# Kernel optimization log

Measured on AMD Instinct MI355X. Metric: run time of the kernel, lower is better.

## Reference

```python
import jax, jax.numpy as jnp
import numpy as np

B, S = 1, 2560
DIM, NH, HD = 1536, 12, 128
F, HH, WW = 4, 20, 32        # F*HH*WW == S (video latent grid)
EPS = 1e-6
C = HD // 2                  # 64 rotary pairs per head
TD = C - 2 * (C // 3)        # 22 temporal rotary dims
SD = C // 3                  # 21 spatial rotary dims (h and w each)


def setup_inputs() -> dict:
    key = jax.random.key(0)
    ks = jax.random.split(key, 4)
    x = jax.random.normal(ks[0], (B, S, DIM), jnp.float32)
    # Wan-style 3D RoPE angle table: angle[pos, j] = pos * inv_freq_j,
    # segments [0:TD]=temporal, [TD:TD+SD]=height, [TD+SD:]=width.
    def inv(n):
        return 1.0 / (10000.0 ** (np.arange(n, dtype=np.float64) / n))
    inv_full = np.concatenate([inv(TD), inv(SD), inv(SD)])
    freqs = jnp.asarray(np.arange(1024)[:, None] * inv_full[None, :], jnp.float32)
    seq_lens = jnp.full((B,), S, jnp.int32)
    grid_sizes = jnp.asarray([[F, HH, WW]], jnp.int32)
    Wqkv = jax.random.normal(ks[1], (DIM, 3 * DIM), jnp.float32) * 0.02
    bqkv = jnp.zeros((3 * DIM,), jnp.float32)
    gq = jnp.ones((DIM,), jnp.float32)
    gk = jnp.ones((DIM,), jnp.float32)
    Wo = jax.random.normal(ks[2], (DIM, DIM), jnp.float32) * 0.02
    bo = jnp.zeros((DIM,), jnp.float32)
    return dict(x=x, seq_lens=seq_lens, grid_sizes=grid_sizes, freqs=freqs,
                Wqkv=Wqkv, bqkv=bqkv, gq=gq, gk=gk, Wo=Wo, bo=bo)


def _rms(x, g):
    xf = x.astype(jnp.float32)
    y = xf * jax.lax.rsqrt(jnp.mean(xf * xf, axis=-1, keepdims=True) + EPS)
    return (y * g).astype(x.dtype)


def _rope3d(x, freqs):
    # x: [B,S,NH,HD]; rotate adjacent (even,odd) pairs by grid-position angles.
    idx = jnp.arange(S)
    f = idx // (HH * WW)
    h = (idx // WW) % HH
    w = idx % WW
    ang = jnp.concatenate([freqs[f, :TD], freqs[h, TD:TD + SD], freqs[w, TD + SD:]], axis=-1)  # [S, C]
    cos = jnp.cos(ang)[None, :, None, :]
    sin = jnp.sin(ang)[None, :, None, :]
    xr, xi = x[..., 0::2], x[..., 1::2]
    out = jnp.stack([xr * cos - xi * sin, xr * sin + xi * cos], axis=-1)
    return out.reshape(x.shape)


def reference(x, seq_lens, grid_sizes, freqs, Wqkv, bqkv, gq, gk, Wo, bo):
    qkv = x @ Wqkv + bqkv                              # [B,S,3*DIM]
    q, k, v = jnp.split(qkv, 3, axis=-1)
    q = _rms(q, gq).reshape(B, S, NH, HD)
    k = _rms(k, gk).reshape(B, S, NH, HD)
    v = v.reshape(B, S, NH, HD)
    q = _rope3d(q, freqs)
    k = _rope3d(k, freqs)
    scores = jnp.einsum('bsnd,btnd->bnst', q, k) / jnp.sqrt(jnp.float32(HD))
    kmask = (jnp.arange(S)[None, :] < seq_lens[:, None])[:, None, None, :]  # k_lens masking
    scores = jnp.where(kmask, scores, jnp.float32(-1e30))
    attn = jax.nn.softmax(scores, axis=-1)
    out = jnp.einsum('bnst,btnd->bsnd', attn, v).reshape(B, S, DIM)
    return out @ Wo + bo
```

## Files before the change

kernel.cpp:

```cpp
#include <hip/hip_runtime.h>
#include <hip/hip_bf16.h>

constexpr int Sq  = 2560;
constexpr int Dm  = 1536;
constexpr int NHe = 12;
constexpr int HDim= 128;
constexpr int N3c = 4608;
constexpr int TDc = 22;
constexpr int SDc = 21;
constexpr int HHc = 20;
constexpr int WWc = 32;

typedef __attribute__((ext_vector_type(4)))  float f32x4;
typedef __attribute__((ext_vector_type(16))) float f32x16;
typedef __attribute__((ext_vector_type(8)))  short bf16x8;
typedef __attribute__((ext_vector_type(4)))  unsigned u32x4;

__device__ __forceinline__ short f2bf(float f) {
  __hip_bfloat16 h = __float2bfloat16(f);
  return __builtin_bit_cast(short, h);
}
__device__ __forceinline__ float bf2f(short s) {
  __hip_bfloat16 h = __builtin_bit_cast(__hip_bfloat16, s);
  return __bfloat162float(h);
}
__device__ __forceinline__ void gll16(const void* g, void* l) {
  __builtin_amdgcn_global_load_lds((const __attribute__((address_space(1))) unsigned int*)g,
                                   (__attribute__((address_space(3))) unsigned int*)l, 16, 0, 0);
}
__device__ __forceinline__ unsigned cvtpk(float lo, float hi) {
  unsigned r;
  asm("v_cvt_pk_bf16_f32 %0, %1, %2" : "=v"(r) : "v"(lo), "v"(hi));
  return r;
}

__global__ __launch_bounds__(256) void k_convert(const float* __restrict__ in,
                                                 short* __restrict__ out, int n4) {
  int i = blockIdx.x * 256 + threadIdx.x;
  if (i >= n4) return;
  float4 v = reinterpret_cast<const float4*>(in)[i];
  short4 o;
  o.x = f2bf(v.x); o.y = f2bf(v.y); o.z = f2bf(v.z); o.w = f2bf(v.w);
  reinterpret_cast<short4*>(out)[i] = o;
}

__global__ void k_transpose_cvt(const float* __restrict__ in, short* __restrict__ out,
                                int R, int C_) {
  __shared__ float tile[32][33];
  int c0 = blockIdx.x * 32, r0 = blockIdx.y * 32;
  int tx = threadIdx.x, ty = threadIdx.y;
#pragma unroll
  for (int i = 0; i < 4; ++i)
    tile[ty + i * 8][tx] = in[(size_t)(r0 + ty + i * 8) * C_ + c0 + tx];
  __syncthreads();
#pragma unroll
  for (int i = 0; i < 4; ++i)
    out[(size_t)(c0 + ty + i * 8) * R + r0 + tx] = f2bf(tile[tx][ty + i * 8]);
}

__global__ void k_transpose_bf16(const short* __restrict__ in, short* __restrict__ out,
                                 int R, int C_) {
  __shared__ short tile[32][34];
  int h = blockIdx.z;
  const short* ih = in + (size_t)h * R * C_;
  short* oh = out + (size_t)h * R * C_;
  int c0 = blockIdx.x * 32, r0 = blockIdx.y * 32;
  int tx = threadIdx.x, ty = threadIdx.y;
#pragma unroll
  for (int i = 0; i < 4; ++i)
    tile[ty + i * 8][tx] = ih[(size_t)(r0 + ty + i * 8) * C_ + c0 + tx];
  __syncthreads();
#pragma unroll
  for (int i = 0; i < 4; ++i)
    oh[(size_t)(c0 + ty + i * 8) * R + r0 + tx] = tile[tx][ty + i * 8];
}

template <int OUT_BF16, int BM, int NTMAJOR>
__global__ __launch_bounds__(256) void k_gemm_bt(const short* __restrict__ A,
                                                 const short* __restrict__ BT,
                                                 const float* __restrict__ bias,
                                                 void* __restrict__ Cp,
                                                 int M, int N, int K, int den) {
  constexpr int MF = BM / 32;
  __shared__ short As[2 * BM * 32];
  __shared__ short Bs[2 * 128 * 32];
  int cpx = gridDim.x >> 3;
  int bid = (blockIdx.x & 7) * cpx + (blockIdx.x >> 3);
  int mt, nt;
  if (NTMAJOR) { mt = bid % den; nt = bid / den; }
  else         { mt = bid / den; nt = bid % den; }
  int tid = threadIdx.x, lane = tid & 63, wid = tid >> 6;
  int wr = wid >> 1, wc = wid & 1;
  f32x4 zero = {0.f, 0.f, 0.f, 0.f};
  f32x4 acc[MF][4];
#pragma unroll
  for (int m = 0; m < MF; ++m)
#pragma unroll
    for (int n = 0; n < 4; ++n) acc[m][n] = zero;

  int lrow = lane >> 2;
  int lk8 = (lane & 3) * 8;
  const size_t arow0 = (size_t)mt * BM, brow0 = (size_t)nt * 128;
  int la = lane & 15, lg = lane >> 4;

  for (int kk = 0; kk < K; kk += 64) {
#pragma unroll
    for (int h = 0; h < 2; ++h) {
#pragma unroll
      for (int i = 0; i < MF / 2; ++i) {
        int rA = (wid * (MF / 2) + i) * 16 + lrow;
        gll16(A + (arow0 + rA) * K + kk + h * 32 + lk8,
              As + h * BM * 32 + rA * 32 + lk8);
      }
#pragma unroll
      for (int i = 0; i < 2; ++i) {
        int rB = (wid * 2 + i) * 16 + lrow;
        gll16(BT + (brow0 + rB) * K + kk + h * 32 + lk8,
              Bs + h * 128 * 32 + rB * 32 + lk8);
      }
    }
    __syncthreads();
#pragma unroll
    for (int h = 0; h < 2; ++h) {
      bf16x8 af[MF], bfr[4];
#pragma unroll
      for (int m = 0; m < MF; ++m)
        af[m] = *(const bf16x8*)(As + h * BM * 32 + (wr * (BM / 2) + m * 16 + la) * 32 + lg * 8);
#pragma unroll
      for (int n = 0; n < 4; ++n)
        bfr[n] = *(const bf16x8*)(Bs + h * 128 * 32 + (wc * 64 + n * 16 + la) * 32 + lg * 8);
#pragma unroll
      for (int m = 0; m < MF; ++m)
#pragma unroll
        for (int n = 0; n < 4; ++n)
          acc[m][n] = __builtin_amdgcn_mfma_f32_16x16x32_bf16(af[m], bfr[n], acc[m][n], 0, 0, 0);
    }
    __syncthreads();
  }
#pragma unroll
  for (int m = 0; m < MF; ++m) {
    int r = (int)arow0 + wr * (BM / 2) + m * 16 + lg * 4;
#pragma unroll
    for (int n = 0; n < 4; ++n) {
      int c = (int)brow0 + wc * 64 + n * 16 + la;
      float b = bias[c];
#pragma unroll
      for (int i = 0; i < 4; ++i) {
        float v = acc[m][n][i] + b;
        if (OUT_BF16) ((short*)Cp)[(size_t)(r + i) * N + c] = f2bf(v);
        else          ((float*)Cp)[(size_t)(r + i) * N + c] = v;
      }
    }
  }
}

__global__ __launch_bounds__(256) void k_rmsrope(const short* __restrict__ qkv,
                                                 const float* __restrict__ freqs,
                                                 const float* __restrict__ gq,
                                                 const float* __restrict__ gk,
                                                 short* __restrict__ Q,
                                                 short* __restrict__ Kx,
                                                 short* __restrict__ V) {
  int s = blockIdx.x;
  const short* row = qkv + (size_t)s * N3c;
  __shared__ float cs[64], sn[64];
  __shared__ float wred[8];
  __shared__ float inv_s[2];
  int tid = threadIdx.x;
  if (tid < 64) {
    int f = s / (HHc * WWc), hh = (s / WWc) % HHc, ww = s % WWc;
    int ridx = tid < TDc ? f : (tid < TDc + SDc ? hh : ww);
    float ang = freqs[ridx * 64 + tid];
    cs[tid] = cosf(ang);
    sn[tid] = sinf(ang);
  }
  float sq = 0.f, sk = 0.f;
  if (tid < 192) {
    bf16x8 a = *(const bf16x8*)(row + tid * 8);
    bf16x8 b = *(const bf16x8*)(row + Dm + tid * 8);
#pragma unroll
    for (int j = 0; j < 8; ++j) {
      float fa = bf2f(a[j]); sq += fa * fa;
      float fb = bf2f(b[j]); sk += fb * fb;
    }
  }
#pragma unroll
  for (int o = 32; o > 0; o >>= 1) { sq += __shfl_down(sq, o); sk += __shfl_down(sk, o); }
  if ((tid & 63) == 0) { wred[tid >> 6] = sq; wred[4 + (tid >> 6)] = sk; }
  __syncthreads();
  if (tid == 0) {
    float a = wred[0] + wred[1] + wred[2] + wred[3];
    float b = wred[4] + wred[5] + wred[6] + wred[7];
    inv_s[0] = rsqrtf(a * (1.0f / Dm) + 1e-6f);
    inv_s[1] = rsqrtf(b * (1.0f / Dm) + 1e-6f);
  }
  __syncthreads();
  float invq = inv_s[0], invk = inv_s[1];
  const float qscale = 0.12751763f;
  for (int p = tid; p < NHe * 64; p += 256) {
    int hd = p >> 6, i = p & 63;
    float c = cs[i], sn_ = sn[i];
    int col = hd * HDim + 2 * i;
    size_t obase = ((size_t)hd * Sq + s) * HDim + 2 * i;
    float xr = bf2f(row[col])     * invq * gq[col];
    float xi = bf2f(row[col + 1]) * invq * gq[col + 1];
    Q[obase]     = f2bf((xr * c - xi * sn_) * qscale);
    Q[obase + 1] = f2bf((xr * sn_ + xi * c) * qscale);
    float yr = bf2f(row[Dm + col])     * invk * gk[col];
    float yi = bf2f(row[Dm + col + 1]) * invk * gk[col + 1];
    Kx[obase]     = f2bf(yr * c - yi * sn_);
    Kx[obase + 1] = f2bf(yr * sn_ + yi * c);
    V[obase]     = row[2 * Dm + col];
    V[obase + 1] = row[2 * Dm + col + 1];
  }
}

__global__ __launch_bounds__(256, 2) void k_attn(const short* __restrict__ Q,
                                                 const short* __restrict__ Kg,
                                                 const short* __restrict__ VT,
                                                 short* __restrict__ O) {
  __shared__ short Xb[2][64 * 128];
  __shared__ short Yb[2][64 * 128];
  __shared__ float Lsh[4][32];
  constexpr int NT = (Sq / 2) / 64;
  int bid = (blockIdx.x & 7) * 60 + (blockIdx.x >> 3);
  int h = bid / 40;
  int q0 = (bid % 40) * 64;
  int tid = threadIdx.x, lane = tid & 63, wid = tid >> 6;
  int qw = wid & 1, kw = wid >> 1;
  int la = lane & 31, hi = lane >> 5;
  const short* Qh = Q  + (size_t)h * Sq * HDim;
  const short* Kh = Kg + (size_t)h * Sq * HDim;
  const short* Vh = VT + (size_t)h * HDim * Sq;
  int qb = q0 + qw * 32;
  int tz = kw * (Sq / 2);
  short* X = Xb[kw];
  short* Y = Yb[kw];

  int koff[8], voff[8], ldo[8];
  const short* Kt = Kh + (size_t)tz * HDim;
  const short* Vt = Vh + tz;
#pragma unroll
  for (int i = 0; i < 8; ++i) {
    int off = (qw * 8 + i) * 1024 + lane * 16;
    int r  = off >> 8, cb  = off & 255;
    koff[i] = r * HDim + ((cb ^ ((r & 15) << 4)) >> 1);
    int r2 = off >> 7, cb2 = off & 127;
    voff[i] = r2 * Sq + ((cb2 ^ ((r2 & 7) << 4)) >> 1);
    ldo[i] = off >> 1;
  }
  auto stageK = [&]() {
#pragma unroll
    for (int i = 0; i < 8; ++i) gll16(Kt + koff[i], X + ldo[i]);
    Kt += 64 * HDim;
  };
  auto stageV = [&]() {
#pragma unroll
    for (int i = 0; i < 8; ++i) gll16(Vt + voff[i], Y + ldo[i]);
    Vt += 64;
  };

  stageK();

  bf16x8 qf[8];
#pragma unroll
  for (int dc = 0; dc < 8; ++dc)
    qf[dc] = *(const bf16x8*)(Qh + (size_t)(qb + la) * HDim + dc * 16 + hi * 8);

  f32x16 o0, o1, o2, o3;
#pragma unroll
  for (int r = 0; r < 16; ++r) { o0[r] = 0.f; o1[r] = 0.f; o2[r] = 0.f; o3[r] = 0.f; }
  float lsum = 0.f;
  const float M2 = 11.5415603f;

  __syncthreads();

  for (int t = 0; t < NT; ++t) {
    stageV();

    f32x16 s0, s1;
#pragma unroll
    for (int r = 0; r < 16; ++r) { s0[r] = 0.f; s1[r] = 0.f; }
    int kcb = ((la & 15) << 4);
#pragma unroll
    for (int dc = 0; dc < 8; ++dc) {
      int bc = (dc * 32 + hi * 16) ^ kcb;
      bf16x8 k0 = *(const bf16x8*)(X + la * 128 + (bc >> 1));
      bf16x8 k1 = *(const bf16x8*)(X + (32 + la) * 128 + (bc >> 1));
      s0 = __builtin_amdgcn_mfma_f32_32x32x16_bf16(k0, qf[dc], s0, 0, 0, 0);
      s1 = __builtin_amdgcn_mfma_f32_32x32x16_bf16(k1, qf[dc], s1, 0, 0, 0);
    }

    float p0[16], p1[16];
#pragma unroll
    for (int r = 0; r < 16; ++r) { p0[r] = exp2f(s0[r] - M2); p1[r] = exp2f(s1[r] - M2); }
    float a0 = 0.f, a1 = 0.f, a2 = 0.f, a3 = 0.f;
#pragma unroll
    for (int m = 0; m < 4; ++m) {
      a0 += p0[m]; a1 += p0[4 + m]; a2 += p0[8 + m]; a3 += p0[12 + m];
      a0 += p1[m]; a1 += p1[4 + m]; a2 += p1[8 + m]; a3 += p1[12 + m];
    }
    lsum += (a0 + a1) + (a2 + a3);

    unsigned w0[8], w1[8];
#pragma unroll
    for (int m = 0; m < 8; ++m) {
      w0[m] = cvtpk(p0[2 * m], p0[2 * m + 1]);
      w1[m] = cvtpk(p1[2 * m], p1[2 * m + 1]);
    }
    unsigned paw[4][4];
#pragma unroll
    for (int tcl = 0; tcl < 2; ++tcl)
#pragma unroll
      for (int jl = 0; jl < 2; ++jl) {
        unsigned A0 = w0[4 * tcl + jl], B0 = w0[4 * tcl + 2 + jl];
        asm("v_permlane32_swap_b32 %0, %1" : "+v"(A0), "+v"(B0));
        paw[tcl][jl] = A0; paw[tcl][2 + jl] = B0;
        unsigned A1 = w1[4 * tcl + jl], B1 = w1[4 * tcl + 2 + jl];
        asm("v_permlane32_swap_b32 %0, %1" : "+v"(A1), "+v"(B1));
        paw[2 + tcl][jl] = A1; paw[2 + tcl][2 + jl] = B1;
      }
    bf16x8 pa[4];
#pragma unroll
    for (int tc = 0; tc < 4; ++tc) {
      u32x4 tw = {paw[tc][0], paw[tc][1], paw[tc][2], paw[tc][3]};
      pa[tc] = __builtin_bit_cast(bf16x8, tw);
    }

    __syncthreads();

    if (t + 1 < NT) stageK();

    int vcb = ((la & 7) << 4);
#pragma unroll
    for (int tc = 0; tc < 4; ++tc) {
      int bc = (tc * 32 + hi * 16) ^ vcb;
      bf16x8 vf0 = *(const bf16x8*)(Y + (la)      * 64 + (bc >> 1));
      bf16x8 vf1 = *(const bf16x8*)(Y + (32 + la) * 64 + (bc >> 1));
      bf16x8 vf2 = *(const bf16x8*)(Y + (64 + la) * 64 + (bc >> 1));
      bf16x8 vf3 = *(const bf16x8*)(Y + (96 + la) * 64 + (bc >> 1));
      o0 = __builtin_amdgcn_mfma_f32_32x32x16_bf16(pa[tc], vf0, o0, 0, 0, 0);
      o1 = __builtin_amdgcn_mfma_f32_32x32x16_bf16(pa[tc], vf1, o1, 0, 0, 0);
      o2 = __builtin_amdgcn_mfma_f32_32x32x16_bf16(pa[tc], vf2, o2, 0, 0, 0);
      o3 = __builtin_amdgcn_mfma_f32_32x32x16_bf16(pa[tc], vf3, o3, 0, 0, 0);
    }
    __syncthreads();
  }

  {
    float A = lsum, B = lsum;
    asm("v_permlane32_swap_b32 %0, %1" : "+v"(A), "+v"(B));
    lsum = A + B;
  }
  if (hi == 0) Lsh[wid][la] = lsum;
  float* fb = (float*)(&Xb[0][0]);
  if (kw == 1) {
    float* dst = fb + qw * 4096 + lane;
#pragma unroll
    for (int r = 0; r < 16; ++r) {
      dst[(r)      * 64] = o0[r];
      dst[(16 + r) * 64] = o1[r];
      dst[(32 + r) * 64] = o2[r];
      dst[(48 + r) * 64] = o3[r];
    }
  }
  __syncthreads();
  if (kw == 0) {
    float ltot = lsum + Lsh[wid + 2][la];
    float rinv = 1.0f / ltot;
    if (hi == 0) Lsh[wid][la] = rinv;
    const float* src = fb + qw * 4096 + lane;
#pragma unroll
    for (int r = 0; r < 16; ++r) {
      o0[r] += src[(r)      * 64];
      o1[r] += src[(16 + r) * 64];
      o2[r] += src[(32 + r) * 64];
      o3[r] += src[(48 + r) * 64];
    }
    float rv[16];
#pragma unroll
    for (int r = 0; r < 16; ++r)
      rv[r] = Lsh[wid][(r & 3) + 8 * (r >> 2) + 4 * hi];
#pragma unroll
    for (int r = 0; r < 16; ++r) {
      int qrow = qb + (r & 3) + 8 * (r >> 2) + 4 * hi;
      short* orow = O + (size_t)qrow * Dm + h * HDim + la;
      orow[0]  = f2bf(o0[r] * rv[r]);
      orow[32] = f2bf(o1[r] * rv[r]);
      orow[64] = f2bf(o2[r] * rv[r]);
      orow[96] = f2bf(o3[r] * rv[r]);
    }
  }
}

extern "C" void kernel_launch(void* const* d_in, const int* in_sizes, int n_in,
                              void* d_out, int out_size, void* d_ws, size_t ws_size,
                              hipStream_t stream) {
  const float* x     = (const float*)d_in[0];
  const float* freqs = (const float*)d_in[3];
  const float* Wqkv  = (const float*)d_in[4];
  const float* bqkv  = (const float*)d_in[5];
  const float* gq    = (const float*)d_in[6];
  const float* gk    = (const float*)d_in[7];
  const float* Wo    = (const float*)d_in[8];
  const float* bo    = (const float*)d_in[9];
  float* out = (float*)d_out;

  char* w = (char*)d_ws;
  short* Qb  = (short*)w;
  short* Kb  = Qb + (size_t)Sq * Dm;
  short* Vb  = Kb + (size_t)Sq * Dm;
  short* xb  = Qb;
  short* WqT = Kb;
  size_t off = (size_t)3 * Sq * Dm * 2;
  short* WoT  = (short*)(w + off); off += (size_t)Dm * Dm * 2;
  short* qkvb = (short*)(w + off); off += (size_t)Sq * N3c * 2;
  short* VTb  = (short*)(w + off); off += (size_t)Sq * Dm * 2;
  short* AOb  = (short*)(w + off); off += (size_t)Sq * Dm * 2;

  dim3 tb(32, 8);
  k_convert<<<(Sq * Dm / 4 + 255) / 256, 256, 0, stream>>>(x, xb, Sq * Dm / 4);
  k_transpose_cvt<<<dim3(N3c / 32, Dm / 32), tb, 0, stream>>>(Wqkv, WqT, Dm, N3c);
  k_transpose_cvt<<<dim3(Dm / 32, Dm / 32), tb, 0, stream>>>(Wo, WoT, Dm, Dm);
  k_gemm_bt<1, 128, 1><<<(Sq / 128) * (N3c / 128), 256, 0, stream>>>(xb, WqT, bqkv, qkvb,
                                                                     Sq, N3c, Dm, Sq / 128);
  k_rmsrope<<<Sq, 256, 0, stream>>>(qkvb, freqs, gq, gk, Qb, Kb, Vb);
  k_transpose_bf16<<<dim3(HDim / 32, Sq / 32, NHe), tb, 0, stream>>>(Vb, VTb, Sq, HDim);
  k_attn<<<480, 256, 0, stream>>>(Qb, Kb, VTb, AOb);
  k_gemm_bt<0, 64, 0><<<(Sq / 64) * (Dm / 128), 256, 0, stream>>>(AOb, WoT, bo, out,
                                                                  Sq, Dm, Dm, Dm / 128);
}
```

Measured before the change: 170.0 us.

## Fuse input conversion and weight transposes into one prep kernel; deepen GEMM k-step

The x-to-bf16 conversion and the two weight transpose-convert kernels are merged into one launch that dispatches on block index. This removes two kernel launches and the gaps between them. The GEMM template gains an NP parameter, so each k-iteration now stages 96 k-values instead of 64, with fewer barriers per K. In exchange, LDS per block grows, which may reduce occupancy, and K=1536 still divides evenly by 96.

```diff
diff --git a/kernel.cpp b/kernel.cpp
--- a/kernel.cpp
+++ b/kernel.cpp
@@ -34,21 +34,37 @@
   return r;
 }
 
-__global__ __launch_bounds__(256) void k_convert(const float* __restrict__ in,
-                                                 short* __restrict__ out, int n4) {
-  int i = blockIdx.x * 256 + threadIdx.x;
-  if (i >= n4) return;
-  float4 v = reinterpret_cast<const float4*>(in)[i];
-  short4 o;
-  o.x = f2bf(v.x); o.y = f2bf(v.y); o.z = f2bf(v.z); o.w = f2bf(v.w);
-  reinterpret_cast<short4*>(out)[i] = o;
-}
-
-__global__ void k_transpose_cvt(const float* __restrict__ in, short* __restrict__ out,
-                                int R, int C_) {
+constexpr int NCONV = Sq * Dm / 4 / 256;
+constexpr int NW1x  = N3c / 32;
+constexpr int NW1   = NW1x * (Dm / 32);
+constexpr int NW2x  = Dm / 32;
+constexpr int NW2   = NW2x * (Dm / 32);
+__global__ __launch_bounds__(256) void k_prep(const float* __restrict__ x,
+                                              short* __restrict__ xb,
+                                              const float* __restrict__ Wq,
+                                              short* __restrict__ WqT,
+                                              const float* __restrict__ Wo,
+                                              short* __restrict__ WoT) {
+  int b = blockIdx.x, tid = threadIdx.x;
+  if (b < NCONV) {
+    int i = b * 256 + tid;
+    float4 v = reinterpret_cast<const float4*>(x)[i];
+    short4 o;
+    o.x = f2bf(v.x); o.y = f2bf(v.y); o.z = f2bf(v.z); o.w = f2bf(v.w);
+    reinterpret_cast<short4*>(xb)[i] = o;
+    return;
+  }
   __shared__ float tile[32][33];
-  int c0 = blockIdx.x * 32, r0 = blockIdx.y * 32;
-  int tx = threadIdx.x, ty = threadIdx.y;
+  const float* in; short* out; int R, C_, bx, by;
+  if (b < NCONV + NW1) {
+    int bb = b - NCONV;
+    in = Wq; out = WqT; R = Dm; C_ = N3c; bx = bb % NW1x; by = bb / NW1x;
+  } else {
+    int bb = b - NCONV - NW1;
+    in = Wo; out = WoT; R = Dm; C_ = Dm; bx = bb % NW2x; by = bb / NW2x;
+  }
+  int c0 = bx * 32, r0 = by * 32;
+  int tx = tid & 31, ty = tid >> 5;
 #pragma unroll
   for (int i = 0; i < 4; ++i)
     tile[ty + i * 8][tx] = in[(size_t)(r0 + ty + i * 8) * C_ + c0 + tx];
@@ -75,15 +91,15 @@
     oh[(size_t)(c0 + ty + i * 8) * R + r0 + tx] = tile[tx][ty + i * 8];
 }
 
-template <int OUT_BF16, int BM, int NTMAJOR>
+template <int OUT_BF16, int BM, int NTMAJOR, int NP>
 __global__ __launch_bounds__(256) void k_gemm_bt(const short* __restrict__ A,
                                                  const short* __restrict__ BT,
                                                  const float* __restrict__ bias,
                                                  void* __restrict__ Cp,
                                                  int M, int N, int K, int den) {
   constexpr int MF = BM / 32;
-  __shared__ short As[2 * BM * 32];
-  __shared__ short Bs[2 * 128 * 32];
+  __shared__ short As[NP * BM * 32];
+  __shared__ short Bs[NP * 128 * 32];
   int cpx = gridDim.x >> 3;
   int bid = (blockIdx.x & 7) * cpx + (blockIdx.x >> 3);
   int mt, nt;
@@ -103,9 +119,9 @@
   const size_t arow0 = (size_t)mt * BM, brow0 = (size_t)nt * 128;
   int la = lane & 15, lg = lane >> 4;
 
-  for (int kk = 0; kk < K; kk += 64) {
-#pragma unroll
-    for (int h = 0; h < 2; ++h) {
+  for (int kk = 0; kk < K; kk += 32 * NP) {
+#pragma unroll
+    for (int h = 0; h < NP; ++h) {
 #pragma unroll
       for (int i = 0; i < MF / 2; ++i) {
         int rA = (wid * (MF / 2) + i) * 16 + lrow;
@@ -121,7 +137,7 @@
     }
     __syncthreads();
 #pragma unroll
-    for (int h = 0; h < 2; ++h) {
+    for (int h = 0; h < NP; ++h) {
       bf16x8 af[MF], bfr[4];
 #pragma unroll
       for (int m = 0; m < MF; ++m)
@@ -419,14 +435,12 @@
   short* AOb  = (short*)(w + off); off += (size_t)Sq * Dm * 2;
 
   dim3 tb(32, 8);
-  k_convert<<<(Sq * Dm / 4 + 255) / 256, 256, 0, stream>>>(x, xb, Sq * Dm / 4);
-  k_transpose_cvt<<<dim3(N3c / 32, Dm / 32), tb, 0, stream>>>(Wqkv, WqT, Dm, N3c);
-  k_transpose_cvt<<<dim3(Dm / 32, Dm / 32), tb, 0, stream>>>(Wo, WoT, Dm, Dm);
-  k_gemm_bt<1, 128, 1><<<(Sq / 128) * (N3c / 128), 256, 0, stream>>>(xb, WqT, bqkv, qkvb,
-                                                                     Sq, N3c, Dm, Sq / 128);
+  k_prep<<<NCONV + NW1 + NW2, 256, 0, stream>>>(x, xb, Wqkv, WqT, Wo, WoT);
+  k_gemm_bt<1, 128, 1, 3><<<(Sq / 128) * (N3c / 128), 256, 0, stream>>>(xb, WqT, bqkv, qkvb,
+                                                                        Sq, N3c, Dm, Sq / 128);
   k_rmsrope<<<Sq, 256, 0, stream>>>(qkvb, freqs, gq, gk, Qb, Kb, Vb);
   k_transpose_bf16<<<dim3(HDim / 32, Sq / 32, NHe), tb, 0, stream>>>(Vb, VTb, Sq, HDim);
   k_attn<<<480, 256, 0, stream>>>(Qb, Kb, VTb, AOb);
-  k_gemm_bt<0, 64, 0><<<(Sq / 64) * (Dm / 128), 256, 0, stream>>>(AOb, WoT, bo, out,
-                                                                  Sq, Dm, Dm, Dm / 128);
-}
+  k_gemm_bt<0, 64, 0, 3><<<(Sq / 64) * (Dm / 128), 256, 0, stream>>>(AOb, WoT, bo, out,
+                                                                     Sq, Dm, Dm, Dm / 128);
+}
```

After: 174.2 us. +2.5%, slower.
